# Kernel tuning notes

Hardware: AMD Instinct MI355X
Metric: run time of the kernel (lower is better)

The kernel has to match this reference:

```python
import jax, jax.numpy as jnp
import numpy as np

BASE_THETA = 0.5
K_DOP = 0.2
K_NOR = 0.15
K_SERO = 0.1
DIM = 1024


def setup_inputs() -> dict:
    key = jax.random.key(0)
    ks = jax.random.split(key, 9)
    scale = 1.0 / np.sqrt(DIM)
    x = jax.random.normal(ks[0], (2, 2048, DIM), dtype=jnp.float32)
    Wq = jax.random.normal(ks[1], (DIM, DIM), dtype=jnp.float32) * scale
    bq = jnp.zeros((DIM,), dtype=jnp.float32)
    Wk = jax.random.normal(ks[2], (DIM, DIM), dtype=jnp.float32) * scale
    bk = jnp.zeros((DIM,), dtype=jnp.float32)
    Wv = jax.random.normal(ks[3], (DIM, DIM), dtype=jnp.float32) * scale
    bv = jnp.zeros((DIM,), dtype=jnp.float32)
    Wo = jax.random.normal(ks[4], (DIM, DIM), dtype=jnp.float32) * scale
    bo = jnp.zeros((DIM,), dtype=jnp.float32)
    return {"x": x, "Wq": Wq, "bq": bq, "Wk": Wk, "bk": bk,
            "Wv": Wv, "bv": bv, "Wo": Wo, "bo": bo}


def reference(x, Wq, bq, Wk, bk, Wv, bv, Wo, bo):
    # Projections: torch nn.Linear computes x @ W.T + b
    q = jnp.einsum('bsd,ed->bse', x, Wq) + bq
    k = jnp.einsum('bsd,ed->bse', x, Wk) + bk
    v = jnp.einsum('bsd,ed->bse', x, Wv) + bv
    # Full [B, S, S] scores (no 1/sqrt(d) scaling in the original)
    qk = jnp.einsum('bsd,btd->bst', q, k)
    theta = (BASE_THETA
             + K_DOP * jax.nn.sigmoid(qk)
             + K_NOR * jnp.tanh(qk)
             + K_SERO * jax.nn.relu(qk))
    attn = jax.nn.softmax(theta, axis=-1)
    out = jnp.einsum('bst,btd->bsd', attn, v)
    return jnp.einsum('bsd,ed->bse', out, Wo) + bo
```

## Files before the change

kernel.cpp:

```cpp
#include <hip/hip_runtime.h>
#include <hip/hip_fp16.h>
#include <stdint.h>

typedef _Float16 f16;
typedef __attribute__((ext_vector_type(8))) _Float16 f16x8;
typedef __attribute__((ext_vector_type(4))) _Float16 f16x4;
typedef __attribute__((ext_vector_type(4))) float f32x4;

#define SEQ 2048
#define DIM 1024
#define NBATCH 2
#define MTOT 4096

__global__ void fill_kernel(float* p, float v, int n){
  int i = blockIdx.x * 256 + threadIdx.x;
  if (i < n) p[i] = v;
}

__global__ void cvt_all(const float* __restrict__ x, const float* __restrict__ Wq,
                        const float* __restrict__ Wk, const float* __restrict__ Wv,
                        const float* __restrict__ Wo,
                        f16* __restrict__ x16, f16* __restrict__ Wcat, f16* __restrict__ Wo16){
  int b = blockIdx.x;
  const float* src; f16* dst; int i;
  if (b < 4096){
    src = x; dst = x16; i = b * 256 + threadIdx.x;
  } else {
    int t = (b - 4096) >> 10;
    i = ((b - 4096) & 1023) * 256 + threadIdx.x;
    src = t == 0 ? Wq : t == 1 ? Wk : t == 2 ? Wv : Wo;
    dst = (t == 3) ? Wo16 : Wcat + (size_t)t * DIM * DIM;
  }
  float4 v = ((const float4*)src)[i];
  ((f16x4*)dst)[i] = (f16x4){(f16)v.x, (f16)v.y, (f16)v.z, (f16)v.w};
}

#define GLOAD16(SRC, DST) __builtin_amdgcn_global_load_lds( \
    (__attribute__((address_space(1))) void*)(SRC), \
    (__attribute__((address_space(3))) void*)(DST), 16, 0, 0)

__device__ __forceinline__ float theta_exp(float v){
  const float e1 = __expf(-v);
  const float sg = 1.f / (1.f + e1);
  const float e2 = e1 * e1;
  const float th = 2.f / (1.f + e2) - 1.f;
  const float theta = 0.5f + 0.2f * sg + 0.15f * th + 0.1f * fmaxf(v, 0.f);
  return __expf(fminf(theta - 10.f, 11.f));
}

__global__ __launch_bounds__(256, 3)
void gemm_qkv(const f16* __restrict__ A0, const f16* __restrict__ B0,
              f16* __restrict__ Oq, f16* __restrict__ Ok, f16* __restrict__ Ov,
              const float* __restrict__ c0, const float* __restrict__ c1,
              const float* __restrict__ c2)
{
  __shared__ __align__(16) f16 As[8192];
  __shared__ __align__(16) f16 Bs[8192];
  const int tid  = threadIdx.x;
  const int lane = tid & 63;
  const int wid  = tid >> 6;
  const int r = blockIdx.x;
  const int x = r & 7, i5 = r >> 3;
  const int bm = (x & 3) * 8 + (i5 & 7);
  const int bn = (x >> 2) * 12 + (i5 >> 3);

  const int s_r  = tid >> 3;
  const int s_cb = (tid & 7) ^ (s_r & 7);
  const f16* Ab = A0 + (long)(bm * 128 + s_r) * DIM + s_cb * 8;
  const f16* Bb = B0 + (long)(bn * 128 + s_r) * DIM + s_cb * 8;

  const int l15 = lane & 15, l7 = lane & 7, lhi = lane >> 4;
  const int wrow = (wid >> 1) * 64;
  const int wcol = (wid & 1) * 64;
  const int ar = (wrow + l15) * 64;
  const int br = (wcol + l15) * 64;
  const int cb0 = ((0 + lhi) ^ l7) * 8;
  const int cb1 = ((4 + lhi) ^ l7) * 8;

  f32x4 acc[4][4] = {};

#pragma unroll
  for (int t = 0; t < 16; ++t){
    __syncthreads();
    GLOAD16(Ab + (long)t*64,                  &As[       tid*8]);
    GLOAD16(Ab + (long)t*64 + (long)32 * DIM, &As[2048 + tid*8]);
    GLOAD16(Ab + (long)t*64 + (long)64 * DIM, &As[4096 + tid*8]);
    GLOAD16(Ab + (long)t*64 + (long)96 * DIM, &As[6144 + tid*8]);
    GLOAD16(Bb + (long)t*64,                  &Bs[       tid*8]);
    GLOAD16(Bb + (long)t*64 + (long)32 * DIM, &Bs[2048 + tid*8]);
    GLOAD16(Bb + (long)t*64 + (long)64 * DIM, &Bs[4096 + tid*8]);
    GLOAD16(Bb + (long)t*64 + (long)96 * DIM, &Bs[6144 + tid*8]);
    __syncthreads();
    f16x8 af[4], bf[4];
#pragma unroll
    for (int i = 0; i < 4; i++) af[i] = *(const f16x8*)&As[ar + i * 1024 + cb0];
#pragma unroll
    for (int j = 0; j < 4; j++) bf[j] = *(const f16x8*)&Bs[br + j * 1024 + cb0];
#pragma unroll
    for (int i = 0; i < 4; i++)
#pragma unroll
      for (int j = 0; j < 4; j++)
        acc[i][j] = __builtin_amdgcn_mfma_f32_16x16x32_f16(af[i], bf[j], acc[i][j], 0, 0, 0);
#pragma unroll
    for (int i = 0; i < 4; i++) af[i] = *(const f16x8*)&As[ar + i * 1024 + cb1];
#pragma unroll
    for (int j = 0; j < 4; j++) bf[j] = *(const f16x8*)&Bs[br + j * 1024 + cb1];
#pragma unroll
    for (int i = 0; i < 4; i++)
#pragma unroll
      for (int j = 0; j < 4; j++)
        acc[i][j] = __builtin_amdgcn_mfma_f32_16x16x32_f16(af[i], bf[j], acc[i][j], 0, 0, 0);
  }

  const int cc = l15;
  const int rr = lhi * 4;
#pragma unroll
  for (int i = 0; i < 4; i++)
#pragma unroll
    for (int j = 0; j < 4; j++){
      const int col = bn * 128 + wcol + j * 16 + cc;
      f16* dst; int dcol; float badd;
      if (col < 1024){       dst = Oq; dcol = col;        badd = c0[dcol]; }
      else if (col < 2048){  dst = Ok; dcol = col - 1024; badd = c1[dcol]; }
      else {                 dst = Ov; dcol = col - 2048; badd = c2[dcol]; }
#pragma unroll
      for (int rq = 0; rq < 4; rq++){
        const int row = bm * 128 + wrow + i * 16 + rr + rq;
        dst[(long)row * DIM + dcol] = (f16)(acc[i][j][rq] + badd);
      }
    }
}

__global__ __launch_bounds__(256, 3)
void gemm_merged(const f16* __restrict__ qbuf, const f16* __restrict__ kbuf,
                 const f16* __restrict__ vbuf, const f16* __restrict__ Wo16,
                 f16* __restrict__ Pbuf, f16* __restrict__ vWoT)
{
  __shared__ __align__(16) f16 As[8192];
  __shared__ __align__(16) f16 Bs[8192];
  const int tid  = threadIdx.x;
  const int lane = tid & 63;
  const int wid  = tid >> 6;
  const int l15 = lane & 15, l7 = lane & 7, lhi = lane >> 4;
  const int s_r  = tid >> 3;
  const int s_cb = (tid & 7) ^ (s_r & 7);
  const int cb0 = ((0 + lhi) ^ l7) * 8;
  const int cb1 = ((4 + lhi) ^ l7) * 8;
  const int cc = l15, rr = lhi * 4;
  const int wrow = (wid >> 1) * 64;
  const int wcol = (wid & 1) * 64;
  const int ar = (wrow + l15) * 64;
  const int br = (wcol + l15) * 64;
  const int r = blockIdx.x;

  const f16 *Ab, *Bb;
  int bm, bn, bz;
  bool isQK;
  if (r < 512){
    isQK = true;
    const int x = r & 7, i5 = r >> 3;
    bz = x >> 2;
    bn = (x & 3) * 4 + (i5 & 3);
    bm = i5 >> 2;
    Ab = qbuf + (long)bz * SEQ * DIM + (long)(bm * 128 + s_r) * DIM + s_cb * 8;
    Bb = kbuf + (long)bz * SEQ * DIM + (long)(bn * 128 + s_r) * DIM + s_cb * 8;
  } else {
    isQK = false;
    const int rr2 = r - 512;
    const int x = rr2 & 7, i5 = rr2 >> 3;
    bz = x >> 2;
    bn = (x & 3) * 2 + (i5 & 1);
    bm = i5 >> 1;
    Ab = vbuf + (long)bz * SEQ * DIM + (long)(bm * 128 + s_r) * DIM + s_cb * 8;
    Bb = Wo16 + (long)(bn * 128 + s_r) * DIM + s_cb * 8;
  }

  f32x4 acc[4][4] = {};

#pragma unroll
  for (int t = 0; t < 16; ++t){
    __syncthreads();
    GLOAD16(Ab + (long)t*64,                  &As[       tid*8]);
    GLOAD16(Ab + (long)t*64 + (long)32 * DIM, &As[2048 + tid*8]);
    GLOAD16(Ab + (long)t*64 + (long)64 * DIM, &As[4096 + tid*8]);
    GLOAD16(Ab + (long)t*64 + (long)96 * DIM, &As[6144 + tid*8]);
    GLOAD16(Bb + (long)t*64,                  &Bs[       tid*8]);
    GLOAD16(Bb + (long)t*64 + (long)32 * DIM, &Bs[2048 + tid*8]);
    GLOAD16(Bb + (long)t*64 + (long)64 * DIM, &Bs[4096 + tid*8]);
    GLOAD16(Bb + (long)t*64 + (long)96 * DIM, &Bs[6144 + tid*8]);
    __syncthreads();
    f16x8 af[4], bf[4];
#pragma unroll
    for (int i = 0; i < 4; i++) af[i] = *(const f16x8*)&As[ar + i * 1024 + cb0];
#pragma unroll
    for (int j = 0; j < 4; j++) bf[j] = *(const f16x8*)&Bs[br + j * 1024 + cb0];
#pragma unroll
    for (int i = 0; i < 4; i++)
#pragma unroll
      for (int j = 0; j < 4; j++)
        acc[i][j] = __builtin_amdgcn_mfma_f32_16x16x32_f16(af[i], bf[j], acc[i][j], 0, 0, 0);
#pragma unroll
    for (int i = 0; i < 4; i++) af[i] = *(const f16x8*)&As[ar + i * 1024 + cb1];
#pragma unroll
    for (int j = 0; j < 4; j++) bf[j] = *(const f16x8*)&Bs[br + j * 1024 + cb1];
#pragma unroll
    for (int i = 0; i < 4; i++)
#pragma unroll
      for (int j = 0; j < 4; j++)
        acc[i][j] = __builtin_amdgcn_mfma_f32_16x16x32_f16(af[i], bf[j], acc[i][j], 0, 0, 0);
  }

  if (isQK){
#pragma unroll
    for (int i = 0; i < 4; i++)
#pragma unroll
      for (int rq = 0; rq < 4; rq++){
        const int row = bm * 128 + wrow + i * 16 + rr + rq;
#pragma unroll
        for (int j = 0; j < 4; j++){
          const int col = bn * 128 + wcol + j * 16 + cc;
          Pbuf[(long)bz * SEQ * SEQ + (long)row * SEQ + col] = (f16)theta_exp(acc[i][j][rq]);
        }
      }
  } else {
#pragma unroll
    for (int i = 0; i < 4; i++)
#pragma unroll
      for (int j = 0; j < 4; j++){
        const int col = bn * 128 + wcol + j * 16 + cc;
        const int row0 = bm * 128 + wrow + i * 16 + rr;
        f16x4 pk = {(f16)acc[i][j][0], (f16)acc[i][j][1],
                    (f16)acc[i][j][2], (f16)acc[i][j][3]};
        *(f16x4*)&vWoT[(long)bz * DIM * SEQ + (long)col * SEQ + row0] = pk;
      }
  }
}

__global__ __launch_bounds__(256, 4)
void gemm_final(const f16* __restrict__ Pb, const f16* __restrict__ Vw,
                f16* __restrict__ psum, float* __restrict__ rowsum)
{
  __shared__ __align__(16) f16 As[8192];
  __shared__ __align__(16) f16 Bs[8192];
  const int tid  = threadIdx.x;
  const int lane = tid & 63;
  const int wid  = tid >> 6;
  const int bm = blockIdx.x, bn = blockIdx.y;
  const int bz = blockIdx.z >> 1, kh = blockIdx.z & 1;

  const f16* Ag = Pb + (long)bz * SEQ * SEQ + (long)kh * 1024;
  const f16* Bg = Vw + (long)bz * DIM * SEQ + (long)kh * 1024;

  const int s_r  = tid >> 3;
  const int s_cb = (tid & 7) ^ (s_r & 7);
  const f16* Ab = Ag + (long)(bm * 128 + s_r) * 2048 + s_cb * 8;
  const f16* Bb = Bg + (long)(bn * 128 + s_r) * 2048 + s_cb * 8;

  const int l15 = lane & 15, l7 = lane & 7, lhi = lane >> 4;
  const int wrow = (wid >> 1) * 64;
  const int wcol = (wid & 1) * 64;
  const int ar = (wrow + l15) * 64;
  const int br = (wcol + l15) * 64;
  const int cb0 = ((0 + lhi) ^ l7) * 8;
  const int cb1 = ((4 + lhi) ^ l7) * 8;
  const bool do_rs = ((wid & 1) == 0);

  f32x4 acc[4][4] = {};
  float rsum[4] = {0.f, 0.f, 0.f, 0.f};

#pragma unroll
  for (int t = 0; t < 16; ++t){
    __syncthreads();
    GLOAD16(Ab + (long)t*64,                   &As[       tid*8]);
    GLOAD16(Ab + (long)t*64 + (long)32 * 2048, &As[2048 + tid*8]);
    GLOAD16(Ab + (long)t*64 + (long)64 * 2048, &As[4096 + tid*8]);
    GLOAD16(Ab + (long)t*64 + (long)96 * 2048, &As[6144 + tid*8]);
    GLOAD16(Bb + (long)t*64,                   &Bs[       tid*8]);
    GLOAD16(Bb + (long)t*64 + (long)32 * 2048, &Bs[2048 + tid*8]);
    GLOAD16(Bb + (long)t*64 + (long)64 * 2048, &Bs[4096 + tid*8]);
    GLOAD16(Bb + (long)t*64 + (long)96 * 2048, &Bs[6144 + tid*8]);
    __syncthreads();
    f16x8 af[4], bf[4];
#pragma unroll
    for (int i = 0; i < 4; i++) af[i] = *(const f16x8*)&As[ar + i * 1024 + cb0];
#pragma unroll
    for (int j = 0; j < 4; j++) bf[j] = *(const f16x8*)&Bs[br + j * 1024 + cb0];
#pragma unroll
    for (int i = 0; i < 4; i++)
#pragma unroll
      for (int j = 0; j < 4; j++)
        acc[i][j] = __builtin_amdgcn_mfma_f32_16x16x32_f16(af[i], bf[j], acc[i][j], 0, 0, 0);
    if (do_rs){
#pragma unroll
      for (int i = 0; i < 4; i++)
#pragma unroll
        for (int e = 0; e < 8; e++) rsum[i] += (float)af[i][e];
    }
#pragma unroll
    for (int i = 0; i < 4; i++) af[i] = *(const f16x8*)&As[ar + i * 1024 + cb1];
#pragma unroll
    for (int j = 0; j < 4; j++) bf[j] = *(const f16x8*)&Bs[br + j * 1024 + cb1];
#pragma unroll
    for (int i = 0; i < 4; i++)
#pragma unroll
      for (int j = 0; j < 4; j++)
        acc[i][j] = __builtin_amdgcn_mfma_f32_16x16x32_f16(af[i], bf[j], acc[i][j], 0, 0, 0);
    if (do_rs){
#pragma unroll
      for (int i = 0; i < 4; i++)
#pragma unroll
        for (int e = 0; e < 8; e++) rsum[i] += (float)af[i][e];
    }
  }

  if (do_rs){
#pragma unroll
    for (int i = 0; i < 4; i++){
      rsum[i] += __shfl_xor(rsum[i], 16, 64);
      rsum[i] += __shfl_xor(rsum[i], 32, 64);
    }
    if (bn == 0 && lane < 16){
#pragma unroll
      for (int i = 0; i < 4; i++)
        rowsum[(long)kh * MTOT + bz * SEQ + bm * 128 + wrow + i * 16 + lane] = rsum[i];
    }
  }

  const int cc = l15;
  const int rr = lhi * 4;
  f16* Po = psum + (long)kh * MTOT * DIM + (long)bz * SEQ * DIM;
#pragma unroll
  for (int i = 0; i < 4; i++)
#pragma unroll
    for (int j = 0; j < 4; j++){
      const int col = bn * 128 + wcol + j * 16 + cc;
#pragma unroll
      for (int r = 0; r < 4; r++){
        const int row = bm * 128 + wrow + i * 16 + rr + r;
        Po[(long)row * DIM + col] = (f16)acc[i][j][r];
      }
    }
}

__global__ __launch_bounds__(256)
void combine_kernel(const f16* __restrict__ psum, const float* __restrict__ rowsum,
                    const float* __restrict__ bo, float* __restrict__ out)
{
  const long i = (long)blockIdx.x * 256 + threadIdx.x;
  const int row = (int)(i >> 8);
  const int c4  = (int)(i & 255);
  f16x4 a = ((const f16x4*)psum)[i];
  f16x4 b = ((const f16x4*)(psum + (long)MTOT * DIM))[i];
  float4 bb = ((const float4*)bo)[c4];
  const float inv = 1.f / (rowsum[row] + rowsum[MTOT + row]);
  float4 o;
  o.x = ((float)a[0] + (float)b[0]) * inv + bb.x;
  o.y = ((float)a[1] + (float)b[1]) * inv + bb.y;
  o.z = ((float)a[2] + (float)b[2]) * inv + bb.z;
  o.w = ((float)a[3] + (float)b[3]) * inv + bb.w;
  ((float4*)out)[i] = o;
}

extern "C" void kernel_launch(void* const* d_in, const int* in_sizes, int n_in,
                              void* d_out, int out_size, void* d_ws, size_t ws_size,
                              hipStream_t stream){
  const float* x  = (const float*)d_in[0];
  const float* Wq = (const float*)d_in[1];
  const float* bq = (const float*)d_in[2];
  const float* Wk = (const float*)d_in[3];
  const float* bk = (const float*)d_in[4];
  const float* Wv = (const float*)d_in[5];
  const float* bv = (const float*)d_in[6];
  const float* Wo = (const float*)d_in[7];
  const float* bo = (const float*)d_in[8];
  float* out = (float*)d_out;

  char* ws = (char*)d_ws;
  size_t off = 0;
  auto alloc = [&](size_t bytes) -> char* {
    char* p = ws + off; off += (bytes + 255) & ~(size_t)255; return p;
  };

  f16* x16     = (f16*)alloc(2ull * MTOT * DIM);
  f16* Wcat    = (f16*)alloc(2ull * 3 * DIM * DIM);
  f16* Wo16    = (f16*)alloc(2ull * DIM * DIM);
  f16* qbuf    = (f16*)alloc(2ull * MTOT * DIM);
  f16* kbuf    = (f16*)alloc(2ull * MTOT * DIM);
  f16* vbuf    = (f16*)alloc(2ull * MTOT * DIM);
  f16* Pbuf    = (f16*)alloc(2ull * NBATCH * SEQ * SEQ);
  f16* vWoT    = (f16*)alloc(2ull * NBATCH * DIM * SEQ);
  f16* psum    = (f16*)alloc(2ull * 2 * MTOT * DIM);
  float* rowsm = (float*)alloc(4ull * 2 * MTOT);

  if (off > ws_size){
    fill_kernel<<<(out_size + 255) / 256, 256, 0, stream>>>(out, 12345.0f, out_size);
    return;
  }

  cvt_all<<<8192, 256, 0, stream>>>(x, Wq, Wk, Wv, Wo, x16, Wcat, Wo16);

  gemm_qkv<<<768, 256, 0, stream>>>(x16, Wcat, qbuf, kbuf, vbuf, bq, bk, bv);

  gemm_merged<<<768, 256, 0, stream>>>(qbuf, kbuf, vbuf, Wo16, Pbuf, vWoT);

  gemm_final<<<dim3(SEQ / 128, DIM / 128, 2 * NBATCH), 256, 0, stream>>>(
      Pbuf, vWoT, psum, rowsm);

  combine_kernel<<<MTOT * DIM / 4 / 256, 256, 0, stream>>>(psum, rowsm, bo, out);
}
```

Measured before the change: 116.4 us.

## Split P and V buffers by K-half and remap final GEMM grid

The intermediate P (exp-theta scores) and transposed vWo buffers are split into two separate contiguous halves along the reduction dimension, so each split-K block of the final GEMM reads rows with a 1024-element stride instead of 2048. The final GEMM is launched as a 1D grid with a custom block-to-tile mapping that interleaves batch/K-half across consecutive blocks, with the aim of improving L2/MALL locality and spreading work across XCDs. Indexing in the producer kernel is adjusted to write into the split buffers. The math is unchanged; the risk is a mapping error or less favourable cache behaviour.

```diff
diff --git a/kernel.cpp b/kernel.cpp
--- a/kernel.cpp
+++ b/kernel.cpp
@@ -134,7 +134,8 @@
 __global__ __launch_bounds__(256, 3)
 void gemm_merged(const f16* __restrict__ qbuf, const f16* __restrict__ kbuf,
                  const f16* __restrict__ vbuf, const f16* __restrict__ Wo16,
-                 f16* __restrict__ Pbuf, f16* __restrict__ vWoT)
+                 f16* __restrict__ P0, f16* __restrict__ P1,
+                 f16* __restrict__ V0, f16* __restrict__ V1)
 {
   __shared__ __align__(16) f16 As[8192];
   __shared__ __align__(16) f16 Bs[8192];
@@ -211,6 +212,7 @@
   }
 
   if (isQK){
+    f16* Ph = (bn < 8) ? P0 : P1;
 #pragma unroll
     for (int i = 0; i < 4; i++)
 #pragma unroll
@@ -219,10 +221,12 @@
 #pragma unroll
         for (int j = 0; j < 4; j++){
           const int col = bn * 128 + wcol + j * 16 + cc;
-          Pbuf[(long)bz * SEQ * SEQ + (long)row * SEQ + col] = (f16)theta_exp(acc[i][j][rq]);
+          Ph[(long)bz * SEQ * 1024 + (long)row * 1024 + (col & 1023)] =
+              (f16)theta_exp(acc[i][j][rq]);
         }
       }
   } else {
+    f16* Vh = (bm < 8) ? V0 : V1;
 #pragma unroll
     for (int i = 0; i < 4; i++)
 #pragma unroll
@@ -231,13 +235,14 @@
         const int row0 = bm * 128 + wrow + i * 16 + rr;
         f16x4 pk = {(f16)acc[i][j][0], (f16)acc[i][j][1],
                     (f16)acc[i][j][2], (f16)acc[i][j][3]};
-        *(f16x4*)&vWoT[(long)bz * DIM * SEQ + (long)col * SEQ + row0] = pk;
+        *(f16x4*)&Vh[(long)bz * DIM * 1024 + (long)col * 1024 + (row0 & 1023)] = pk;
       }
   }
 }
 
 __global__ __launch_bounds__(256, 4)
-void gemm_final(const f16* __restrict__ Pb, const f16* __restrict__ Vw,
+void gemm_final(const f16* __restrict__ P0, const f16* __restrict__ P1,
+                const f16* __restrict__ V0, const f16* __restrict__ V1,
                 f16* __restrict__ psum, float* __restrict__ rowsum)
 {
   __shared__ __align__(16) f16 As[8192];
@@ -245,16 +250,20 @@
   const int tid  = threadIdx.x;
   const int lane = tid & 63;
   const int wid  = tid >> 6;
-  const int bm = blockIdx.x, bn = blockIdx.y;
-  const int bz = blockIdx.z >> 1, kh = blockIdx.z & 1;
-
-  const f16* Ag = Pb + (long)bz * SEQ * SEQ + (long)kh * 1024;
-  const f16* Bg = Vw + (long)bz * DIM * SEQ + (long)kh * 1024;
+  const int r = blockIdx.x;
+  const int x = r & 7, i5 = r >> 3;
+  const int z4 = x >> 1;
+  const int bz = z4 >> 1, kh = z4 & 1;
+  const int bn = (x & 1) * 4 + (i5 & 3);
+  const int bm = i5 >> 2;
+
+  const f16* Ag = (kh ? P1 : P0) + (long)bz * SEQ * 1024;
+  const f16* Bg = (kh ? V1 : V0) + (long)bz * DIM * 1024;
 
   const int s_r  = tid >> 3;
   const int s_cb = (tid & 7) ^ (s_r & 7);
-  const f16* Ab = Ag + (long)(bm * 128 + s_r) * 2048 + s_cb * 8;
-  const f16* Bb = Bg + (long)(bn * 128 + s_r) * 2048 + s_cb * 8;
+  const f16* Ab = Ag + (long)(bm * 128 + s_r) * 1024 + s_cb * 8;
+  const f16* Bb = Bg + (long)(bn * 128 + s_r) * 1024 + s_cb * 8;
 
   const int l15 = lane & 15, l7 = lane & 7, lhi = lane >> 4;
   const int wrow = (wid >> 1) * 64;
@@ -272,13 +281,13 @@
   for (int t = 0; t < 16; ++t){
     __syncthreads();
     GLOAD16(Ab + (long)t*64,                   &As[       tid*8]);
-    GLOAD16(Ab + (long)t*64 + (long)32 * 2048, &As[2048 + tid*8]);
-    GLOAD16(Ab + (long)t*64 + (long)64 * 2048, &As[4096 + tid*8]);
-    GLOAD16(Ab + (long)t*64 + (long)96 * 2048, &As[6144 + tid*8]);
+    GLOAD16(Ab + (long)t*64 + (long)32 * 1024, &As[2048 + tid*8]);
+    GLOAD16(Ab + (long)t*64 + (long)64 * 1024, &As[4096 + tid*8]);
+    GLOAD16(Ab + (long)t*64 + (long)96 * 1024, &As[6144 + tid*8]);
     GLOAD16(Bb + (long)t*64,                   &Bs[       tid*8]);
-    GLOAD16(Bb + (long)t*64 + (long)32 * 2048, &Bs[2048 + tid*8]);
-    GLOAD16(Bb + (long)t*64 + (long)64 * 2048, &Bs[4096 + tid*8]);
-    GLOAD16(Bb + (long)t*64 + (long)96 * 2048, &Bs[6144 + tid*8]);
+    GLOAD16(Bb + (long)t*64 + (long)32 * 1024, &Bs[2048 + tid*8]);
+    GLOAD16(Bb + (long)t*64 + (long)64 * 1024, &Bs[4096 + tid*8]);
+    GLOAD16(Bb + (long)t*64 + (long)96 * 1024, &Bs[6144 + tid*8]);
     __syncthreads();
     f16x8 af[4], bf[4];
 #pragma unroll
@@ -335,9 +344,9 @@
     for (int j = 0; j < 4; j++){
       const int col = bn * 128 + wcol + j * 16 + cc;
 #pragma unroll
-      for (int r = 0; r < 4; r++){
-        const int row = bm * 128 + wrow + i * 16 + rr + r;
-        Po[(long)row * DIM + col] = (f16)acc[i][j][r];
+      for (int rq = 0; rq < 4; rq++){
+        const int row = bm * 128 + wrow + i * 16 + rr + rq;
+        Po[(long)row * DIM + col] = (f16)acc[i][j][rq];
       }
     }
 }
@@ -387,8 +396,10 @@
   f16* qbuf    = (f16*)alloc(2ull * MTOT * DIM);
   f16* kbuf    = (f16*)alloc(2ull * MTOT * DIM);
   f16* vbuf    = (f16*)alloc(2ull * MTOT * DIM);
-  f16* Pbuf    = (f16*)alloc(2ull * NBATCH * SEQ * SEQ);
-  f16* vWoT    = (f16*)alloc(2ull * NBATCH * DIM * SEQ);
+  f16* P0      = (f16*)alloc(2ull * NBATCH * SEQ * 1024);
+  f16* P1      = (f16*)alloc(2ull * NBATCH * SEQ * 1024);
+  f16* V0      = (f16*)alloc(2ull * NBATCH * DIM * 1024);
+  f16* V1      = (f16*)alloc(2ull * NBATCH * DIM * 1024);
   f16* psum    = (f16*)alloc(2ull * 2 * MTOT * DIM);
   float* rowsm = (float*)alloc(4ull * 2 * MTOT);
 
@@ -401,10 +412,9 @@
 
   gemm_qkv<<<768, 256, 0, stream>>>(x16, Wcat, qbuf, kbuf, vbuf, bq, bk, bv);
 
-  gemm_merged<<<768, 256, 0, stream>>>(qbuf, kbuf, vbuf, Wo16, Pbuf, vWoT);
-
-  gemm_final<<<dim3(SEQ / 128, DIM / 128, 2 * NBATCH), 256, 0, stream>>>(
-      Pbuf, vWoT, psum, rowsm);
+  gemm_merged<<<768, 256, 0, stream>>>(qbuf, kbuf, vbuf, Wo16, P0, P1, V0, V1);
+
+  gemm_final<<<512, 256, 0, stream>>>(P0, P1, V0, V1, psum, rowsm);
 
   combine_kernel<<<MTOT * DIM / 4 / 256, 256, 0, stream>>>(psum, rowsm, bo, out);
 }
```

New measurement: 115.9 us, median of 2. No clear change (-0.4%).
